# Optimization experiments

Measured on AMD Instinct MI355X. Metric: run time of the kernel, lower is better.

Reference implementation:

```python
import jax, jax.numpy as jnp
import numpy as np
from math import sqrt

B, P, D = 4, 2048, 1024
H, DK = 16, 64  # n_heads, d_keys


def setup_inputs() -> dict:
    key = jax.random.key(0)
    ks = jax.random.split(key, 6)
    s = 1.0 / sqrt(D)
    return {
        "target_embedding": jax.random.normal(ks[0], (B, P, D), dtype=jnp.float32),
        "Wq": jax.random.normal(ks[1], (D, H * DK), dtype=jnp.float32) * s,
        "bq": jnp.zeros((H * DK,), dtype=jnp.float32),
        "Wk": jax.random.normal(ks[2], (D, H * DK), dtype=jnp.float32) * s,
        "bk": jnp.zeros((H * DK,), dtype=jnp.float32),
        "Wv": jax.random.normal(ks[3], (D, H * DK), dtype=jnp.float32) * s,
        "bv": jnp.zeros((H * DK,), dtype=jnp.float32),
        "Wo": jax.random.normal(ks[4], (H * DK, D), dtype=jnp.float32) * s,
        "bo": jnp.zeros((D,), dtype=jnp.float32),
    }


def reference(target_embedding, Wq, bq, Wk, bk, Wv, bv, Wo, bo):
    x = target_embedding
    b, p, _ = x.shape
    # QKV projections -> [B, P, H, DK]
    q = (x @ Wq + bq).reshape(b, p, H, DK)
    k = (x @ Wk + bk).reshape(b, p, H, DK)
    v = (x @ Wv + bv).reshape(b, p, H, DK)
    scale = 1.0 / sqrt(DK)
    scores = jnp.einsum("bphd,bqhd->bhpq", q, k)  # [B, H, P, P]
    A = jax.nn.softmax(scale * scores, axis=-1)  # dropout is identity in eval
    rep = jnp.einsum("bhpq,bqhd->bphd", A, v).reshape(b, p, H * DK)
    return rep @ Wo + bo
```

## Files before the change

kernel.cpp:

```cpp
#include <hip/hip_runtime.h>

typedef __attribute__((ext_vector_type(8))) short short8;
typedef __attribute__((ext_vector_type(4))) short short4v;
typedef __attribute__((ext_vector_type(4))) float f32x4;
typedef __attribute__((ext_vector_type(4))) unsigned short ushort4v;
typedef __attribute__((ext_vector_type(2))) unsigned int uint2v;

#define GLOBAL_AS __attribute__((address_space(1)))
#define LDS_AS    __attribute__((address_space(3)))

__device__ __forceinline__ unsigned short f2bf(float f) {
    unsigned int u = __float_as_uint(f);
    u += 0x7fffu + ((u >> 16) & 1u);
    return (unsigned short)(u >> 16);
}

__device__ __forceinline__ unsigned int pack_rhu(float a, float b) {
    unsigned int ua = __float_as_uint(a) + 0x8000u;
    unsigned int ub = __float_as_uint(b) + 0x8000u;
    return __builtin_amdgcn_perm(ub, ua, 0x07060302u);
}

__device__ __forceinline__ short4v pack4_rhu(float p0, float p1, float p2, float p3) {
    uint2v uu;
    uu[0] = pack_rhu(p0, p1);
    uu[1] = pack_rhu(p2, p3);
    return __builtin_bit_cast(short4v, uu);
}

__device__ __forceinline__ float fexp2(float x) {
    return __builtin_amdgcn_exp2f(x);
}

__device__ __forceinline__ void async_cp16(void* lds, const void* g) {
    __builtin_amdgcn_global_load_lds((GLOBAL_AS unsigned int*)g,
                                     (LDS_AS unsigned int*)lds, 16, 0, 0);
}

#define SCL2E 0.18033688011112042591999058512524f

__global__ void prep_kernel(const float* __restrict__ X,
                            const float* __restrict__ Wq,
                            const float* __restrict__ Wk,
                            const float* __restrict__ Wv,
                            const float* __restrict__ Wo,
                            unsigned short* __restrict__ Xb,
                            unsigned short* __restrict__ Wts) {
    const int z = blockIdx.z;
    if (z < 4) {
        __shared__ float tile[32][33];
        const float* src = (z == 0) ? Wq : (z == 1) ? Wk : (z == 2) ? Wv : Wo;
        unsigned short* dst = Wts + z * 1048576;
        const int tx = threadIdx.x, ty = threadIdx.y;
        const int x0 = blockIdx.x * 32, y0 = blockIdx.y * 32;
#pragma unroll
        for (int i = 0; i < 32; i += 8)
            tile[ty + i][tx] = src[(y0 + ty + i) * 1024 + x0 + tx];
        __syncthreads();
#pragma unroll
        for (int i = 0; i < 32; i += 8)
            dst[(x0 + ty + i) * 1024 + y0 + tx] = f2bf(tile[tx][ty + i]);
    } else {
        const int tid = threadIdx.y * 32 + threadIdx.x;
        const int chunk = blockIdx.y * 32 + blockIdx.x;
        const int base = chunk * 8192;
#pragma unroll
        for (int pass = 0; pass < 8; ++pass) {
            int i = base + pass * 1024 + tid * 4;
            float4 v = *(const float4*)&X[i];
            ushort4v o;
            o.x = f2bf(v.x); o.y = f2bf(v.y); o.z = f2bf(v.z); o.w = f2bf(v.w);
            *(ushort4v*)&Xb[i] = o;
        }
    }
}

__global__ void transpose_v_kernel(const unsigned short* __restrict__ V,
                                   unsigned short* __restrict__ Vt) {
    __shared__ unsigned short tile[32][33];
    const int bh = blockIdx.z;
    const int p0 = blockIdx.x * 32, d0 = blockIdx.y * 32;
    const unsigned short* src = V + bh * (2048 * 64);
    unsigned short* dst = Vt + bh * (2048 * 64);
    const int tx = threadIdx.x, ty = threadIdx.y;
#pragma unroll
    for (int i = 0; i < 32; i += 8)
        tile[ty + i][tx] = src[(p0 + ty + i) * 64 + d0 + tx];
    __syncthreads();
#pragma unroll
    for (int i = 0; i < 32; i += 8)
        dst[(d0 + ty + i) * 2048 + p0 + tx] = tile[tx][ty + i];
}

__device__ __forceinline__ void gemm_mainloop_128(
    const unsigned short* __restrict__ A, const unsigned short* __restrict__ Bt,
    int m0, int n0, unsigned short* As, unsigned short* Bs, f32x4 acc[4][4]) {
    const int tid = threadIdx.x;
    const int lane = tid & 63;
    const int wave = tid >> 6;
    const int wr = wave >> 1, wc = wave & 1;
    const int c = lane & 15, quad = lane >> 4;

#pragma unroll
    for (int mt = 0; mt < 4; ++mt)
#pragma unroll
        for (int nt = 0; nt < 4; ++nt)
            acc[mt][nt] = (f32x4)0.0f;

    for (int k0 = 0; k0 < 1024; k0 += 32) {
#pragma unroll
        for (int i = 0; i < 2; ++i) {
            int s = tid + 256 * i;
            int r = s >> 2, gp = s & 3;
            int g = gp ^ ((r >> 1) & 3);
            async_cp16(&As[s * 8], &A[(m0 + r) * 1024 + k0 + g * 8]);
        }
#pragma unroll
        for (int i = 0; i < 2; ++i) {
            int s = tid + 256 * i;
            int r = s >> 2, gp = s & 3;
            int g = gp ^ ((r >> 1) & 3);
            async_cp16(&Bs[s * 8], &Bt[(n0 + r) * 1024 + k0 + g * 8]);
        }
        asm volatile("s_waitcnt vmcnt(0)" ::: "memory");
        __syncthreads();

        short8 af[4], bf[4];
#pragma unroll
        for (int mt = 0; mt < 4; ++mt) {
            int r = wr * 64 + mt * 16 + c;
            int gp = quad ^ ((r >> 1) & 3);
            af[mt] = *(const short8*)&As[r * 32 + gp * 8];
        }
#pragma unroll
        for (int nt = 0; nt < 4; ++nt) {
            int r = wc * 64 + nt * 16 + c;
            int gp = quad ^ ((r >> 1) & 3);
            bf[nt] = *(const short8*)&Bs[r * 32 + gp * 8];
        }
#pragma unroll
        for (int mt = 0; mt < 4; ++mt)
#pragma unroll
            for (int nt = 0; nt < 4; ++nt)
                acc[mt][nt] = __builtin_amdgcn_mfma_f32_16x16x32_bf16(
                    af[mt], bf[nt], acc[mt][nt], 0, 0, 0);
        __syncthreads();
    }
}

__global__ __launch_bounds__(256, 3) void gemm_qkv_kernel(
    const unsigned short* __restrict__ Xb, const unsigned short* __restrict__ Wts,
    const float* __restrict__ bq, const float* __restrict__ bk,
    const float* __restrict__ bv, unsigned short* __restrict__ Qb,
    unsigned short* __restrict__ Kb, unsigned short* __restrict__ Vb) {
    __shared__ __align__(16) unsigned short As[128 * 32];
    __shared__ __align__(16) unsigned short Bs[128 * 32];
    const int z = blockIdx.z;
    const unsigned short* Bt = Wts + z * 1048576;
    const float* bias = (z == 0) ? bq : (z == 1) ? bk : bv;
    const int m0 = blockIdx.y * 128, n0 = blockIdx.x * 128;
    f32x4 acc[4][4];
    gemm_mainloop_128(Xb, Bt, m0, n0, As, Bs, acc);

    const int lane = threadIdx.x & 63, wave = threadIdx.x >> 6;
    const int wr = wave >> 1, wc = wave & 1;
    const int c = lane & 15, quad = lane >> 4;
    unsigned short* dst = (z == 0) ? Qb : (z == 1) ? Kb : Vb;
    const float qscale = (z == 0) ? SCL2E : 1.0f;
#pragma unroll
    for (int nt = 0; nt < 4; ++nt) {
        int col = n0 + wc * 64 + nt * 16 + c;
        float bb = bias[col];
        int h = col >> 6, dk = col & 63;
#pragma unroll
        for (int mt = 0; mt < 4; ++mt) {
#pragma unroll
            for (int r = 0; r < 4; ++r) {
                int row = m0 + wr * 64 + mt * 16 + quad * 4 + r;
                int b = row >> 11, p = row & 2047;
                float v = (acc[mt][nt][r] + bb) * qscale;
                dst[((b * 16 + h) * 2048 + p) * 64 + dk] = f2bf(v);
            }
        }
    }
}

__device__ __forceinline__ void load_kv_regs(
    const unsigned short* __restrict__ Kbh, const unsigned short* __restrict__ Vbh,
    int k0, int tid, short8 kr[2], short8 vr[2]) {
#pragma unroll
    for (int i = 0; i < 2; ++i) {
        int s = tid + 256 * i;
        int r = s >> 3, gp = s & 7;
        int g = gp ^ (r & 7);
        kr[i] = *(const short8*)&Kbh[(k0 + r) * 64 + g * 8];
        vr[i] = *(const short8*)&Vbh[r * 2048 + k0 + g * 8];
    }
}

__global__ __launch_bounds__(256, 2) void attn_kernel(
    const unsigned short* __restrict__ Q, const unsigned short* __restrict__ K,
    const unsigned short* __restrict__ Vt, unsigned short* __restrict__ rep) {
    __shared__ __align__(16) unsigned short SMEM[16384];
    const int tid = threadIdx.x, lane = tid & 63, wave = tid >> 6;
    const int c = lane & 15, quad = lane >> 4;
    const int bh = blockIdx.y;
    const int q0 = blockIdx.x * 256 + wave * 64;
    const unsigned short* Qbh = Q + bh * (2048 * 64);
    const unsigned short* Kbh = K + bh * (2048 * 64);
    const unsigned short* Vbh = Vt + bh * (64 * 2048);

    short8 qf[4][2];
#pragma unroll
    for (int t = 0; t < 4; ++t)
#pragma unroll
        for (int ks = 0; ks < 2; ++ks)
            qf[t][ks] = *(const short8*)&Qbh[(q0 + t * 16 + c) * 64 + ks * 32 + quad * 8];

    short8 kr[2], vr[2];
    load_kv_regs(Kbh, Vbh, 0, tid, kr, vr);

    f32x4 o[4][4];
    float lpart[4] = {0.0f, 0.0f, 0.0f, 0.0f};
#pragma unroll
    for (int t = 0; t < 4; ++t)
#pragma unroll
        for (int d = 0; d < 4; ++d) o[t][d] = (f32x4)0.0f;

    for (int it = 0; it < 32; ++it) {
        const int buf = it & 1;
        unsigned short* Ksb = &SMEM[buf * 4096];
        unsigned short* Vsb = &SMEM[8192 + buf * 4096];
#pragma unroll
        for (int i = 0; i < 2; ++i) {
            int s = tid + 256 * i;
            *(short8*)&Ksb[s * 8] = kr[i];
            *(short8*)&Vsb[s * 8] = vr[i];
        }
        __syncthreads();
        if (it < 31)
            load_kv_regs(Kbh, Vbh, (it + 1) * 64, tid, kr, vr);

        short8 kf[4][2];
#pragma unroll
        for (int nt = 0; nt < 4; ++nt)
#pragma unroll
            for (int ks = 0; ks < 2; ++ks) {
                int r = nt * 16 + c;
                int gp2 = (quad + 4 * ks) ^ (r & 7);
                kf[nt][ks] = *(const short8*)&Ksb[r * 64 + gp2 * 8];
            }

        short4v pfrag[4][4];
#pragma unroll
        for (int t = 0; t < 4; ++t) {
#pragma unroll
            for (int nt = 0; nt < 4; ++nt) {
                f32x4 z4 = (f32x4)0.0f;
                z4 = __builtin_amdgcn_mfma_f32_16x16x32_bf16(kf[nt][0], qf[t][0], z4, 0, 0, 0);
                z4 = __builtin_amdgcn_mfma_f32_16x16x32_bf16(kf[nt][1], qf[t][1], z4, 0, 0, 0);
                float p0 = fexp2(z4[0]), p1 = fexp2(z4[1]);
                float p2 = fexp2(z4[2]), p3 = fexp2(z4[3]);
                lpart[t] += (p0 + p1) + (p2 + p3);
                pfrag[nt][t] = pack4_rhu(p0, p1, p2, p3);
            }
        }

#pragma unroll
        for (int dkt = 0; dkt < 4; ++dkt) {
            int r = dkt * 16 + c;
#pragma unroll
            for (int kt = 0; kt < 4; ++kt) {
                int gbase = 2 * kt + (quad >> 1);
                int g = gbase ^ (r & 7);
                int eloff = g * 8 + (quad & 1) * 4;
                short4v vf4 = *(const short4v*)&Vsb[r * 64 + eloff];
#pragma unroll
                for (int t = 0; t < 4; ++t)
                    o[t][dkt] = __builtin_amdgcn_mfma_f32_16x16x16bf16_1k(
                        vf4, pfrag[kt][t], o[t][dkt], 0, 0, 0);
            }
        }
    }

    float inv[4];
#pragma unroll
    for (int t = 0; t < 4; ++t) {
        float l = lpart[t];
        l += __shfl_xor(l, 16);
        l += __shfl_xor(l, 32);
        inv[t] = 1.0f / l;
    }

    __syncthreads();
    const int b = bh >> 4, h = bh & 15;
    unsigned short* ob = &SMEM[wave * 2304];
#pragma unroll
    for (int pass = 0; pass < 2; ++pass) {
#pragma unroll
        for (int th = 0; th < 2; ++th) {
            int t = pass * 2 + th;
#pragma unroll
            for (int dkt = 0; dkt < 4; ++dkt) {
                short4v frag = pack4_rhu(o[t][dkt][0] * inv[t], o[t][dkt][1] * inv[t],
                                         o[t][dkt][2] * inv[t], o[t][dkt][3] * inv[t]);
                *(short4v*)&ob[(th * 16 + c) * 72 + dkt * 16 + quad * 4] = frag;
            }
        }
        asm volatile("s_waitcnt lgkmcnt(0)" ::: "memory");
#pragma unroll
        for (int sp = 0; sp < 4; ++sp) {
            int qr = sp * 8 + (lane >> 3);
            int d8 = (lane & 7) * 8;
            short8 row = *(const short8*)&ob[qr * 72 + d8];
            *(short8*)&rep[(b * 2048 + q0 + pass * 32 + qr) * 1024 + h * 64 + d8] = row;
        }
    }
}

__global__ __launch_bounds__(256, 3) void gemm_out_kernel(
    const unsigned short* __restrict__ rep, const unsigned short* __restrict__ Wot,
    const float* __restrict__ bo, float* __restrict__ out) {
    __shared__ __align__(16) unsigned short As[128 * 32];
    __shared__ __align__(16) unsigned short Bs[128 * 32];
    const int m0 = blockIdx.y * 128, n0 = blockIdx.x * 128;
    f32x4 acc[4][4];
    gemm_mainloop_128(rep, Wot, m0, n0, As, Bs, acc);
    const int lane = threadIdx.x & 63, wave = threadIdx.x >> 6;
    const int wr = wave >> 1, wc = wave & 1;
    const int c = lane & 15, quad = lane >> 4;
#pragma unroll
    for (int nt = 0; nt < 4; ++nt) {
        int col = n0 + wc * 64 + nt * 16 + c;
        float bb = bo[col];
#pragma unroll
        for (int mt = 0; mt < 4; ++mt) {
            int row = m0 + wr * 64 + mt * 16 + quad * 4;
#pragma unroll
            for (int r = 0; r < 4; ++r)
                out[(row + r) * 1024 + col] = acc[mt][nt][r] + bb;
        }
    }
}

extern "C" void kernel_launch(void* const* d_in, const int* in_sizes, int n_in,
                              void* d_out, int out_size, void* d_ws, size_t ws_size,
                              hipStream_t stream) {
    (void)in_sizes; (void)n_in; (void)out_size; (void)ws_size;
    const float* X  = (const float*)d_in[0];
    const float* Wq = (const float*)d_in[1];
    const float* bq = (const float*)d_in[2];
    const float* Wk = (const float*)d_in[3];
    const float* bk = (const float*)d_in[4];
    const float* Wv = (const float*)d_in[5];
    const float* bv = (const float*)d_in[6];
    const float* Wo = (const float*)d_in[7];
    const float* bo = (const float*)d_in[8];
    float* out = (float*)d_out;

    char* ws = (char*)d_ws;
    unsigned short* Xb   = (unsigned short*)(ws);
    unsigned short* Wts  = (unsigned short*)(ws + (16u << 20));
    unsigned short* Qb   = (unsigned short*)(ws + (24u << 20));
    unsigned short* Kb   = (unsigned short*)(ws + (40u << 20));
    unsigned short* Vb   = (unsigned short*)(ws + (56u << 20));
    unsigned short* Vtb  = (unsigned short*)(ws);
    unsigned short* repb = (unsigned short*)(ws + (56u << 20));

    prep_kernel<<<dim3(32, 32, 5), dim3(32, 8), 0, stream>>>(X, Wq, Wk, Wv, Wo, Xb, Wts);
    gemm_qkv_kernel<<<dim3(8, 64, 3), 256, 0, stream>>>(Xb, Wts, bq, bk, bv, Qb, Kb, Vb);
    transpose_v_kernel<<<dim3(64, 2, 64), dim3(32, 8), 0, stream>>>(Vb, Vtb);
    attn_kernel<<<dim3(8, 64), 256, 0, stream>>>(Qb, Kb, Vtb, repb);
    gemm_out_kernel<<<dim3(8, 64), 256, 0, stream>>>(repb, Wts + 3 * 1048576, bo, out);
}
```

Baseline: 297.8 us.

## Split attention keys across wave pairs with async LDS staging and more blocks

The attention kernel now gives each block 128 queries instead of 256. Its four waves form two query groups times two key halves, and the partial outputs and row sums are combined through LDS at the end. K/V tiles are copied straight into double-buffered LDS with async 16-byte copies instead of passing through registers. Launch bounds rise to 4 blocks per CU and the grid doubles, which aims to raise occupancy and latency hiding. The cost is an extra cross-wave reduction with several barriers, and half the waves sit idle during the epilogue.

```diff
diff --git a/kernel.cpp b/kernel.cpp
--- a/kernel.cpp
+++ b/kernel.cpp
@@ -185,27 +185,28 @@
     }
 }
 
-__device__ __forceinline__ void load_kv_regs(
+__device__ __forceinline__ void stage_kv_async(
     const unsigned short* __restrict__ Kbh, const unsigned short* __restrict__ Vbh,
-    int k0, int tid, short8 kr[2], short8 vr[2]) {
+    int k0, int tid, unsigned short* Ksb, unsigned short* Vsb) {
 #pragma unroll
     for (int i = 0; i < 2; ++i) {
         int s = tid + 256 * i;
         int r = s >> 3, gp = s & 7;
         int g = gp ^ (r & 7);
-        kr[i] = *(const short8*)&Kbh[(k0 + r) * 64 + g * 8];
-        vr[i] = *(const short8*)&Vbh[r * 2048 + k0 + g * 8];
-    }
-}
-
-__global__ __launch_bounds__(256, 2) void attn_kernel(
+        async_cp16(&Ksb[s * 8], &Kbh[(k0 + r) * 64 + g * 8]);
+        async_cp16(&Vsb[s * 8], &Vbh[r * 2048 + k0 + g * 8]);
+    }
+}
+
+__global__ __launch_bounds__(256, 4) void attn_kernel(
     const unsigned short* __restrict__ Q, const unsigned short* __restrict__ K,
     const unsigned short* __restrict__ Vt, unsigned short* __restrict__ rep) {
     __shared__ __align__(16) unsigned short SMEM[16384];
     const int tid = threadIdx.x, lane = tid & 63, wave = tid >> 6;
     const int c = lane & 15, quad = lane >> 4;
+    const int wq = wave & 1, wk = wave >> 1;
     const int bh = blockIdx.y;
-    const int q0 = blockIdx.x * 256 + wave * 64;
+    const int q0 = blockIdx.x * 128 + wq * 64;
     const unsigned short* Qbh = Q + bh * (2048 * 64);
     const unsigned short* Kbh = K + bh * (2048 * 64);
     const unsigned short* Vbh = Vt + bh * (64 * 2048);
@@ -217,8 +218,7 @@
         for (int ks = 0; ks < 2; ++ks)
             qf[t][ks] = *(const short8*)&Qbh[(q0 + t * 16 + c) * 64 + ks * 32 + quad * 8];
 
-    short8 kr[2], vr[2];
-    load_kv_regs(Kbh, Vbh, 0, tid, kr, vr);
+    stage_kv_async(Kbh, Vbh, 0, tid, &SMEM[0], &SMEM[8192]);
 
     f32x4 o[4][4];
     float lpart[4] = {0.0f, 0.0f, 0.0f, 0.0f};
@@ -231,68 +231,91 @@
         const int buf = it & 1;
         unsigned short* Ksb = &SMEM[buf * 4096];
         unsigned short* Vsb = &SMEM[8192 + buf * 4096];
-#pragma unroll
-        for (int i = 0; i < 2; ++i) {
-            int s = tid + 256 * i;
-            *(short8*)&Ksb[s * 8] = kr[i];
-            *(short8*)&Vsb[s * 8] = vr[i];
-        }
+        asm volatile("s_waitcnt vmcnt(0)" ::: "memory");
         __syncthreads();
         if (it < 31)
-            load_kv_regs(Kbh, Vbh, (it + 1) * 64, tid, kr, vr);
-
-        short8 kf[4][2];
-#pragma unroll
-        for (int nt = 0; nt < 4; ++nt)
-#pragma unroll
-            for (int ks = 0; ks < 2; ++ks) {
-                int r = nt * 16 + c;
-                int gp2 = (quad + 4 * ks) ^ (r & 7);
-                kf[nt][ks] = *(const short8*)&Ksb[r * 64 + gp2 * 8];
-            }
-
-        short4v pfrag[4][4];
-#pragma unroll
-        for (int t = 0; t < 4; ++t) {
-#pragma unroll
-            for (int nt = 0; nt < 4; ++nt) {
+            stage_kv_async(Kbh, Vbh, (it + 1) * 64, tid,
+                           &SMEM[(buf ^ 1) * 4096], &SMEM[8192 + (buf ^ 1) * 4096]);
+
+#pragma unroll
+        for (int nt = 0; nt < 2; ++nt) {
+            short8 kf0, kf1;
+            {
+                int r = wk * 32 + nt * 16 + c;
+                kf0 = *(const short8*)&Ksb[r * 64 + ((quad) ^ (r & 7)) * 8];
+                kf1 = *(const short8*)&Ksb[r * 64 + ((quad + 4) ^ (r & 7)) * 8];
+            }
+            short4v vf[4];
+            const int ktg = wk * 2 + nt;
+#pragma unroll
+            for (int dkt = 0; dkt < 4; ++dkt) {
+                int r = dkt * 16 + c;
+                int g = (2 * ktg + (quad >> 1)) ^ (r & 7);
+                vf[dkt] = *(const short4v*)&Vsb[r * 64 + g * 8 + (quad & 1) * 4];
+            }
+#pragma unroll
+            for (int t = 0; t < 4; ++t) {
                 f32x4 z4 = (f32x4)0.0f;
-                z4 = __builtin_amdgcn_mfma_f32_16x16x32_bf16(kf[nt][0], qf[t][0], z4, 0, 0, 0);
-                z4 = __builtin_amdgcn_mfma_f32_16x16x32_bf16(kf[nt][1], qf[t][1], z4, 0, 0, 0);
+                z4 = __builtin_amdgcn_mfma_f32_16x16x32_bf16(kf0, qf[t][0], z4, 0, 0, 0);
+                z4 = __builtin_amdgcn_mfma_f32_16x16x32_bf16(kf1, qf[t][1], z4, 0, 0, 0);
                 float p0 = fexp2(z4[0]), p1 = fexp2(z4[1]);
                 float p2 = fexp2(z4[2]), p3 = fexp2(z4[3]);
                 lpart[t] += (p0 + p1) + (p2 + p3);
-                pfrag[nt][t] = pack4_rhu(p0, p1, p2, p3);
-            }
-        }
-
-#pragma unroll
-        for (int dkt = 0; dkt < 4; ++dkt) {
-            int r = dkt * 16 + c;
-#pragma unroll
-            for (int kt = 0; kt < 4; ++kt) {
-                int gbase = 2 * kt + (quad >> 1);
-                int g = gbase ^ (r & 7);
-                int eloff = g * 8 + (quad & 1) * 4;
-                short4v vf4 = *(const short4v*)&Vsb[r * 64 + eloff];
-#pragma unroll
-                for (int t = 0; t < 4; ++t)
+                short4v pf = pack4_rhu(p0, p1, p2, p3);
+#pragma unroll
+                for (int dkt = 0; dkt < 4; ++dkt)
                     o[t][dkt] = __builtin_amdgcn_mfma_f32_16x16x16bf16_1k(
-                        vf4, pfrag[kt][t], o[t][dkt], 0, 0, 0);
-            }
-        }
-    }
+                        vf[dkt], pf, o[t][dkt], 0, 0, 0);
+            }
+        }
+    }
+
+#pragma unroll
+    for (int t = 0; t < 4; ++t) {
+        lpart[t] += __shfl_xor(lpart[t], 16);
+        lpart[t] += __shfl_xor(lpart[t], 32);
+    }
+
+    float* FS = (float*)SMEM;
+    __syncthreads();
+#pragma unroll
+    for (int p = 0; p < 2; ++p) {
+        if (wk == 1) {
+#pragma unroll
+            for (int tt = 0; tt < 2; ++tt)
+#pragma unroll
+                for (int dkt = 0; dkt < 4; ++dkt) {
+                    int off = (tt * 16 + dkt * 4) ^ ((lane & 7) << 2);
+                    *(f32x4*)&FS[wq * 2048 + lane * 32 + off] = o[p * 2 + tt][dkt];
+                }
+            if (p == 0 && quad == 0) {
+#pragma unroll
+                for (int t = 0; t < 4; ++t) FS[4096 + wq * 64 + t * 16 + c] = lpart[t];
+            }
+        }
+        __syncthreads();
+        if (wk == 0) {
+#pragma unroll
+            for (int tt = 0; tt < 2; ++tt)
+#pragma unroll
+                for (int dkt = 0; dkt < 4; ++dkt) {
+                    int off = (tt * 16 + dkt * 4) ^ ((lane & 7) << 2);
+                    f32x4 v = *(const f32x4*)&FS[wq * 2048 + lane * 32 + off];
+                    o[p * 2 + tt][dkt] += v;
+                }
+            if (p == 0) {
+#pragma unroll
+                for (int t = 0; t < 4; ++t) lpart[t] += FS[4096 + wq * 64 + t * 16 + c];
+            }
+        }
+        __syncthreads();
+    }
+    if (wk != 0) return;
 
     float inv[4];
 #pragma unroll
-    for (int t = 0; t < 4; ++t) {
-        float l = lpart[t];
-        l += __shfl_xor(l, 16);
-        l += __shfl_xor(l, 32);
-        inv[t] = 1.0f / l;
-    }
-
-    __syncthreads();
+    for (int t = 0; t < 4; ++t) inv[t] = 1.0f / lpart[t];
+
     const int b = bh >> 4, h = bh & 15;
     unsigned short* ob = &SMEM[wave * 2304];
 #pragma unroll
@@ -370,6 +393,6 @@
     prep_kernel<<<dim3(32, 32, 5), dim3(32, 8), 0, stream>>>(X, Wq, Wk, Wv, Wo, Xb, Wts);
     gemm_qkv_kernel<<<dim3(8, 64, 3), 256, 0, stream>>>(Xb, Wts, bq, bk, bv, Qb, Kb, Vb);
     transpose_v_kernel<<<dim3(64, 2, 64), dim3(32, 8), 0, stream>>>(Vb, Vtb);
-    attn_kernel<<<dim3(8, 64), 256, 0, stream>>>(Qb, Kb, Vtb, repb);
+    attn_kernel<<<dim3(16, 64), 256, 0, stream>>>(Qb, Kb, Vtb, repb);
     gemm_out_kernel<<<dim3(8, 64), 256, 0, stream>>>(repb, Wts + 3 * 1048576, bo, out);
 }
```

Result: slower. 651.6 us (+118.8%).

## Stage K/V tiles with async global-to-LDS copies and 128-key blocks

Applied to the files above, without the earlier changes.

Replaces the register-staged K/V prefetch with async 16-byte global-to-LDS copies, doubles the key tile to 128 so the loop runs half as many barrier iterations, and interleaves the QK, exp and PV MFMAs per 16-key subtile instead of staging all P fragments first. It also raises wave priority around the PV MFMAs. This aims to cut register pressure, VGPR-to-LDS store traffic and sync overhead. In exchange, LDS use doubles to 64 KB per block, which may limit two blocks per CU, and the swizzle for the wider V tile changes.

```diff
diff --git a/kernel.cpp b/kernel.cpp
--- a/kernel.cpp
+++ b/kernel.cpp
@@ -185,23 +185,29 @@
     }
 }
 
-__device__ __forceinline__ void load_kv_regs(
+__device__ __forceinline__ void stage_kv_async128(
     const unsigned short* __restrict__ Kbh, const unsigned short* __restrict__ Vbh,
-    int k0, int tid, short8 kr[2], short8 vr[2]) {
-#pragma unroll
-    for (int i = 0; i < 2; ++i) {
+    int k0, int tid, unsigned short* Ksb, unsigned short* Vsb) {
+#pragma unroll
+    for (int i = 0; i < 4; ++i) {
         int s = tid + 256 * i;
         int r = s >> 3, gp = s & 7;
         int g = gp ^ (r & 7);
-        kr[i] = *(const short8*)&Kbh[(k0 + r) * 64 + g * 8];
-        vr[i] = *(const short8*)&Vbh[r * 2048 + k0 + g * 8];
+        async_cp16(&Ksb[s * 8], &Kbh[(k0 + r) * 64 + g * 8]);
+    }
+#pragma unroll
+    for (int i = 0; i < 4; ++i) {
+        int s = tid + 256 * i;
+        int r = s >> 4, gp = s & 15;
+        int g = (gp & 8) | ((gp & 7) ^ (r & 7));
+        async_cp16(&Vsb[s * 8], &Vbh[r * 2048 + k0 + g * 8]);
     }
 }
 
 __global__ __launch_bounds__(256, 2) void attn_kernel(
     const unsigned short* __restrict__ Q, const unsigned short* __restrict__ K,
     const unsigned short* __restrict__ Vt, unsigned short* __restrict__ rep) {
-    __shared__ __align__(16) unsigned short SMEM[16384];
+    __shared__ __align__(16) unsigned short SMEM[32768];
     const int tid = threadIdx.x, lane = tid & 63, wave = tid >> 6;
     const int c = lane & 15, quad = lane >> 4;
     const int bh = blockIdx.y;
@@ -217,8 +223,7 @@
         for (int ks = 0; ks < 2; ++ks)
             qf[t][ks] = *(const short8*)&Qbh[(q0 + t * 16 + c) * 64 + ks * 32 + quad * 8];
 
-    short8 kr[2], vr[2];
-    load_kv_regs(Kbh, Vbh, 0, tid, kr, vr);
+    stage_kv_async128(Kbh, Vbh, 0, tid, &SMEM[0], &SMEM[16384]);
 
     f32x4 o[4][4];
     float lpart[4] = {0.0f, 0.0f, 0.0f, 0.0f};
@@ -227,58 +232,47 @@
 #pragma unroll
         for (int d = 0; d < 4; ++d) o[t][d] = (f32x4)0.0f;
 
-    for (int it = 0; it < 32; ++it) {
+    for (int it = 0; it < 16; ++it) {
         const int buf = it & 1;
-        unsigned short* Ksb = &SMEM[buf * 4096];
-        unsigned short* Vsb = &SMEM[8192 + buf * 4096];
-#pragma unroll
-        for (int i = 0; i < 2; ++i) {
-            int s = tid + 256 * i;
-            *(short8*)&Ksb[s * 8] = kr[i];
-            *(short8*)&Vsb[s * 8] = vr[i];
-        }
+        unsigned short* Ksb = &SMEM[buf * 8192];
+        unsigned short* Vsb = &SMEM[16384 + buf * 8192];
+        asm volatile("s_waitcnt vmcnt(0)" ::: "memory");
         __syncthreads();
-        if (it < 31)
-            load_kv_regs(Kbh, Vbh, (it + 1) * 64, tid, kr, vr);
-
-        short8 kf[4][2];
-#pragma unroll
-        for (int nt = 0; nt < 4; ++nt)
-#pragma unroll
-            for (int ks = 0; ks < 2; ++ks) {
+        if (it < 15)
+            stage_kv_async128(Kbh, Vbh, (it + 1) * 128, tid,
+                              &SMEM[(buf ^ 1) * 8192], &SMEM[16384 + (buf ^ 1) * 8192]);
+
+#pragma unroll
+        for (int nt = 0; nt < 8; ++nt) {
+            short8 kf0, kf1;
+            {
                 int r = nt * 16 + c;
-                int gp2 = (quad + 4 * ks) ^ (r & 7);
-                kf[nt][ks] = *(const short8*)&Ksb[r * 64 + gp2 * 8];
-            }
-
-        short4v pfrag[4][4];
-#pragma unroll
-        for (int t = 0; t < 4; ++t) {
-#pragma unroll
-            for (int nt = 0; nt < 4; ++nt) {
+                kf0 = *(const short8*)&Ksb[r * 64 + ((quad) ^ (r & 7)) * 8];
+                kf1 = *(const short8*)&Ksb[r * 64 + ((quad + 4) ^ (r & 7)) * 8];
+            }
+            short4v vf[4];
+#pragma unroll
+            for (int dkt = 0; dkt < 4; ++dkt) {
+                int r = dkt * 16 + c;
+                int raw = nt * 2 + (quad >> 1);
+                int g = (raw & 8) | ((raw ^ (r & 7)) & 7);
+                vf[dkt] = *(const short4v*)&Vsb[r * 128 + g * 8 + (quad & 1) * 4];
+            }
+#pragma unroll
+            for (int t = 0; t < 4; ++t) {
                 f32x4 z4 = (f32x4)0.0f;
-                z4 = __builtin_amdgcn_mfma_f32_16x16x32_bf16(kf[nt][0], qf[t][0], z4, 0, 0, 0);
-                z4 = __builtin_amdgcn_mfma_f32_16x16x32_bf16(kf[nt][1], qf[t][1], z4, 0, 0, 0);
+                z4 = __builtin_amdgcn_mfma_f32_16x16x32_bf16(kf0, qf[t][0], z4, 0, 0, 0);
+                z4 = __builtin_amdgcn_mfma_f32_16x16x32_bf16(kf1, qf[t][1], z4, 0, 0, 0);
                 float p0 = fexp2(z4[0]), p1 = fexp2(z4[1]);
                 float p2 = fexp2(z4[2]), p3 = fexp2(z4[3]);
                 lpart[t] += (p0 + p1) + (p2 + p3);
-                pfrag[nt][t] = pack4_rhu(p0, p1, p2, p3);
-            }
-        }
-
-#pragma unroll
-        for (int dkt = 0; dkt < 4; ++dkt) {
-            int r = dkt * 16 + c;
-#pragma unroll
-            for (int kt = 0; kt < 4; ++kt) {
-                int gbase = 2 * kt + (quad >> 1);
-                int g = gbase ^ (r & 7);
-                int eloff = g * 8 + (quad & 1) * 4;
-                short4v vf4 = *(const short4v*)&Vsb[r * 64 + eloff];
-#pragma unroll
-                for (int t = 0; t < 4; ++t)
+                short4v pf = pack4_rhu(p0, p1, p2, p3);
+                __builtin_amdgcn_s_setprio(1);
+#pragma unroll
+                for (int dkt = 0; dkt < 4; ++dkt)
                     o[t][dkt] = __builtin_amdgcn_mfma_f32_16x16x16bf16_1k(
-                        vf4, pfrag[kt][t], o[t][dkt], 0, 0, 0);
+                        vf[dkt], pf, o[t][dkt], 0, 0, 0);
+                __builtin_amdgcn_s_setprio(0);
             }
         }
     }
```

New measurement: 311.3 us. 4.5% more time.

## Split attention inner loop into two key halves with prioritized PV MFMA blocks

Applied to the files above, without the earlier changes.

Restructures each 64-key tile of the attention loop into two 32-key halves. Each half loads its V fragments and K fragments, computes QK^T with exp2, then runs the PV MFMAs inside sched_barrier fences with raised wave priority. The aim is to shorten register live ranges for K and P fragments and to interleave softmax exp work with MFMA work across waves. The sched barriers limit how freely the compiler can schedule, and the setprio hint may or may not help overlap.

```diff
diff --git a/kernel.cpp b/kernel.cpp
--- a/kernel.cpp
+++ b/kernel.cpp
@@ -241,45 +241,56 @@
         if (it < 31)
             load_kv_regs(Kbh, Vbh, (it + 1) * 64, tid, kr, vr);
 
-        short8 kf[4][2];
-#pragma unroll
-        for (int nt = 0; nt < 4; ++nt)
-#pragma unroll
-            for (int ks = 0; ks < 2; ++ks) {
-                int r = nt * 16 + c;
-                int gp2 = (quad + 4 * ks) ^ (r & 7);
-                kf[nt][ks] = *(const short8*)&Ksb[r * 64 + gp2 * 8];
+#pragma unroll
+        for (int ntp = 0; ntp < 2; ++ntp) {
+            short4v vfp[2][4];
+#pragma unroll
+            for (int ntl = 0; ntl < 2; ++ntl) {
+                const int nt = ntp * 2 + ntl;
+#pragma unroll
+                for (int dkt = 0; dkt < 4; ++dkt) {
+                    int r = dkt * 16 + c;
+                    int gbase = 2 * nt + (quad >> 1);
+                    int g = gbase ^ (r & 7);
+                    int eloff = g * 8 + (quad & 1) * 4;
+                    vfp[ntl][dkt] = *(const short4v*)&Vsb[r * 64 + eloff];
+                }
             }
 
-        short4v pfrag[4][4];
-#pragma unroll
-        for (int t = 0; t < 4; ++t) {
-#pragma unroll
-            for (int nt = 0; nt < 4; ++nt) {
-                f32x4 z4 = (f32x4)0.0f;
-                z4 = __builtin_amdgcn_mfma_f32_16x16x32_bf16(kf[nt][0], qf[t][0], z4, 0, 0, 0);
-                z4 = __builtin_amdgcn_mfma_f32_16x16x32_bf16(kf[nt][1], qf[t][1], z4, 0, 0, 0);
-                float p0 = fexp2(z4[0]), p1 = fexp2(z4[1]);
-                float p2 = fexp2(z4[2]), p3 = fexp2(z4[3]);
-                lpart[t] += (p0 + p1) + (p2 + p3);
-                pfrag[nt][t] = pack4_rhu(p0, p1, p2, p3);
+            short4v pfr[2][4];
+#pragma unroll
+            for (int ntl = 0; ntl < 2; ++ntl) {
+                const int nt = ntp * 2 + ntl;
+                short8 kf0, kf1;
+                {
+                    int r = nt * 16 + c;
+                    kf0 = *(const short8*)&Ksb[r * 64 + ((quad) ^ (r & 7)) * 8];
+                    kf1 = *(const short8*)&Ksb[r * 64 + ((quad + 4) ^ (r & 7)) * 8];
+                }
+#pragma unroll
+                for (int t = 0; t < 4; ++t) {
+                    f32x4 z4 = (f32x4)0.0f;
+                    z4 = __builtin_amdgcn_mfma_f32_16x16x32_bf16(kf0, qf[t][0], z4, 0, 0, 0);
+                    z4 = __builtin_amdgcn_mfma_f32_16x16x32_bf16(kf1, qf[t][1], z4, 0, 0, 0);
+                    float p0 = fexp2(z4[0]), p1 = fexp2(z4[1]);
+                    float p2 = fexp2(z4[2]), p3 = fexp2(z4[3]);
+                    lpart[t] += (p0 + p1) + (p2 + p3);
+                    pfr[ntl][t] = pack4_rhu(p0, p1, p2, p3);
+                }
             }
-        }
-
-#pragma unroll
-        for (int dkt = 0; dkt < 4; ++dkt) {
-            int r = dkt * 16 + c;
-#pragma unroll
-            for (int kt = 0; kt < 4; ++kt) {
-                int gbase = 2 * kt + (quad >> 1);
-                int g = gbase ^ (r & 7);
-                int eloff = g * 8 + (quad & 1) * 4;
-                short4v vf4 = *(const short4v*)&Vsb[r * 64 + eloff];
-#pragma unroll
-                for (int t = 0; t < 4; ++t)
-                    o[t][dkt] = __builtin_amdgcn_mfma_f32_16x16x16bf16_1k(
-                        vf4, pfrag[kt][t], o[t][dkt], 0, 0, 0);
-            }
+
+            __builtin_amdgcn_sched_barrier(0);
+            __builtin_amdgcn_s_setprio(1);
+#pragma unroll
+            for (int t = 0; t < 4; ++t)
+#pragma unroll
+                for (int dkt = 0; dkt < 4; ++dkt)
+#pragma unroll
+                    for (int ntl = 0; ntl < 2; ++ntl)
+                        o[t][dkt] = __builtin_amdgcn_mfma_f32_16x16x16bf16_1k(
+                            vfp[ntl][dkt], pfr[ntl][t], o[t][dkt], 0, 0, 0);
+            __builtin_amdgcn_s_setprio(0);
+            __builtin_amdgcn_sched_barrier(0);
         }
     }
 
```

After: 302.2 us. About the same (+1.5%).
